# Kernel optimization log

Hardware: AMD Instinct MI355X
Metric: run time of the kernel (lower is better)

Reference implementation:

```python
import jax, jax.numpy as jnp
import numpy as np

# dims
B, H, W = 2, 128, 256
MD = 34            # model_dim (last 2 channels = sin/cos lat)
LD = MD - 2        # learnable_dim = 32
NH, HD = 4, 8      # n_heads, head_dim
SH = 64            # shared_hidden (DISCO out channels)
K = 25             # number of DISCO basis functions (5x5 kernel_shape)
P = 7              # local stencil width (lat x lon support of geodesic basis)
R = P // 2
FF1, FF2 = 512, 256


def setup_inputs() -> dict:
    key = jax.random.key(0)
    ks = jax.random.split(key, 16)
    x = jax.random.normal(ks[0], (B, H, W, MD), dtype=jnp.float32)
    # latitude-dependent sparse geodesic basis values over a 7x7 stencil
    psi_val = jax.random.uniform(ks[1], (K, H, P * P), dtype=jnp.float32) * 0.1
    disco_w = jax.random.normal(ks[2], (SH, K), dtype=jnp.float32) * 0.1
    disco_b = jax.random.normal(ks[3], (SH,), dtype=jnp.float32) * 0.01
    # per-head MLP: shared_hidden -> 32 -> 1
    hw1 = jax.random.normal(ks[4], (NH, SH, 32), dtype=jnp.float32) * (1.0 / np.sqrt(SH))
    hb1 = jax.random.normal(ks[5], (NH, 32), dtype=jnp.float32) * 0.01
    hw2 = jax.random.normal(ks[6], (NH, 32, 1), dtype=jnp.float32) * (1.0 / np.sqrt(32))
    hb2 = jax.random.normal(ks[7], (NH, 1), dtype=jnp.float32) * 0.01
    # FFN: model_dim -> 512 -> 256 -> learnable_dim
    fw1 = jax.random.normal(ks[8], (MD, FF1), dtype=jnp.float32) * (1.0 / np.sqrt(MD))
    fw1 = fw1.at[-2:, :].set(0.0)  # matches ffn[0].weight[:, -2:] = 0 init
    fb1 = jax.random.normal(ks[9], (FF1,), dtype=jnp.float32) * 0.01
    fw2 = jax.random.normal(ks[10], (FF1, FF2), dtype=jnp.float32) * (1.0 / np.sqrt(FF1))
    fb2 = jax.random.normal(ks[11], (FF2,), dtype=jnp.float32) * 0.01
    fw3 = jax.random.normal(ks[12], (FF2, LD), dtype=jnp.float32) * (1.0 / np.sqrt(FF2))
    fb3 = jax.random.normal(ks[13], (LD,), dtype=jnp.float32) * 0.01
    return {"x": x, "psi_val": psi_val, "disco_w": disco_w, "disco_b": disco_b,
            "hw1": hw1, "hb1": hb1, "hw2": hw2, "hb2": hb2,
            "fw1": fw1, "fb1": fb1, "fw2": fw2, "fb2": fb2, "fw3": fw3, "fb3": fb3}


def _gelu(t):
    return jax.nn.gelu(t, approximate=False)  # torch nn.GELU default (erf)


def _disco_s2(xn, psi_val, disco_w, disco_b):
    """DISCO sparse-basis conv on single-channel maps.
    xn: (N, H, W). Basis values vary with output latitude, longitude is
    translation-invariant; support is a lat-clamped / lon-wrapped 7x7 stencil.
    Returns (N, SH, H, W)."""
    xp = jnp.pad(xn, ((0, 0), (R, R), (0, 0)), mode="edge")  # clamp at poles
    shifts = []
    for dlat in range(P):
        row = xp[:, dlat:dlat + H, :]
        for dlon in range(-R, R + 1):
            shifts.append(jnp.roll(row, -dlon, axis=2))  # wrap in longitude
    xs = jnp.stack(shifts, axis=1)  # (N, P*P, H, W)
    basis = jnp.einsum("khp,nphw->nkhw", psi_val, xs)       # basis aggregation
    return jnp.einsum("fk,nkhw->nfhw", disco_w, basis) + disco_b[None, :, None, None]


def reference(x, psi_val, disco_w, disco_b, hw1, hb1, hw2, hb2,
              fw1, fb1, fw2, fb2, fw3, fb3):
    x_learn = x[..., :LD]
    sin_cos = x[..., LD:]
    x_res = x_learn
    # (B,H,W,LD) -> (B*LD, H, W): each learnable channel is a 1-channel map
    xn = x_learn.transpose(0, 3, 1, 2).reshape(B * LD, H, W)
    d = _disco_s2(xn, psi_val, disco_w, disco_b)              # (B*LD, SH, H, W)
    d = d.reshape(B, LD, SH, H, W).transpose(0, 3, 4, 1, 2)    # (B,H,W,LD,SH)
    # per-head MLP over its head_dim slice (head index is outer in LD)
    d = d.reshape(B, H, W, NH, HD, SH)
    h = _gelu(jnp.einsum("bxynds,nso->bxyndo", d, hw1) + hb1[None, None, None, :, None, :])
    h = jnp.einsum("bxyndo,noe->bxynde", h, hw2) + hb2[None, None, None, :, None, :]
    x_learn = h[..., 0].reshape(B, H, W, LD)
    x_learn = x_learn + x_res                                  # use_residual
    x_full = jnp.concatenate([x_learn, sin_cos], axis=-1)
    x_res2 = x_learn
    t = _gelu(x_full @ fw1 + fb1)
    t = _gelu(t @ fw2 + fb2)
    t = t @ fw3 + fb3                                          # dropout p=0 -> id
    x_learn = t + x_res2
    return jnp.concatenate([x_learn, sin_cos], axis=-1)
```

## Files before the change

### kernel.cpp

```cpp
#include <hip/hip_runtime.h>
#include <math.h>


typedef __attribute__((ext_vector_type(8))) short bfrag;
typedef __attribute__((ext_vector_type(4))) float ffrag;
typedef __attribute__((ext_vector_type(4))) short short4v;

union bfi4 { int4 i; bfrag b; };

__device__ __forceinline__ float gelu_f(float v) {
  const float z = v * (2.3022077484f + 0.1029451564f * v * v);
  const float e = __builtin_amdgcn_exp2f(-z);
  return v * __builtin_amdgcn_rcpf(1.0f + e);
}

__device__ __forceinline__ short f2bf(float f) {
  union { float f; unsigned u; } v; v.f = f;
  unsigned r = (v.u + 0x7fffu + ((v.u >> 16) & 1u)) >> 16;
  return (short)r;
}

__device__ __forceinline__ short f2bf_fast(float f) {
  union { float f; unsigned u; } v; v.f = f;
  return (short)((v.u + 0x8000u) >> 16);
}

__device__ __forceinline__ float bf2f(short s) {
  union { float f; unsigned u; } v;
  v.u = ((unsigned)(unsigned short)s) << 16;
  return v.f;
}

__device__ __forceinline__ int pkbf(float a, float b) {
  union { float f; unsigned u; } va, vb; va.f = a; vb.f = b;
  return (int)__builtin_amdgcn_perm(vb.u + 0x8000u, va.u + 0x8000u, 0x07060302u);
}

template <int CTRL>
__device__ __forceinline__ float dpp_add(float v) {
  union { float f; int i; } s, t;
  s.f = v;
  t.i = __builtin_amdgcn_update_dpp(0, s.i, CTRL, 0xf, 0xf, true);
  return v + t.f;
}
__device__ __forceinline__ float reduce16(float v) {
  v = dpp_add<0xB1>(v);
  v = dpp_add<0x4E>(v);
  v = dpp_add<0x141>(v);
  v = dpp_add<0x140>(v);
  return v;
}

__device__ __forceinline__ void st4bf(short* p, float4 v) {
  short4v s;
  s[0] = f2bf(v.x); s[1] = f2bf(v.y); s[2] = f2bf(v.z); s[3] = f2bf(v.w);
  *(short4v*)p = s;
}

__global__ __launch_bounds__(256) void k01_prep(
    const float* __restrict__ psi, const float* __restrict__ dw,
    const float* __restrict__ db,
    const float* __restrict__ fw1, const float* __restrict__ fw2,
    const float* __restrict__ fw3, const float* __restrict__ hw1,
    const float* __restrict__ hb1,
    short* __restrict__ wcb, short* __restrict__ fw1s,
    short* __restrict__ fw2s, short* __restrict__ fw3s,
    short* __restrict__ hw1b, float* __restrict__ hb1e) {
  __shared__ __align__(16) char sm[33280];
  const int bid = blockIdx.x;
  const int tid = threadIdx.x;

  if (bid < 128) {
    short* tile = (short*)sm;
    const int h = bid;
    const int lane = tid & 63;
    const int w = __builtin_amdgcn_readfirstlane(tid >> 6);
    float dwreg[25];
#pragma unroll
    for (int kk = 0; kk < 25; ++kk) dwreg[kk] = dw[lane * 25 + kk];
    const int p0 = w * 13;
    const int pend = (p0 + 13 < 49) ? (p0 + 13) : 49;
#pragma unroll 1
    for (int p = p0; p < pend; ++p) {
      float acc = 0.f;
#pragma unroll
      for (int kk = 0; kk < 25; ++kk)
        acc += dwreg[kk] * psi[kk * 6272 + h * 49 + p];
      tile[lane * 52 + p] = f2bf(acc);
    }
    __syncthreads();
    short* outp = wcb + h * 8192;
    for (int idx = tid; idx < 8192; idx += 256) {
      const int jj = idx & 7, ln = (idx >> 3) & 63;
      const int nt = (idx >> 9) & 3, kt = (idx >> 11) & 1, par = idx >> 12;
      const int k = kt * 32 + (ln >> 4) * 8 + jj;
      const int f = nt * 16 + (ln & 15);
      const int r = k >> 3, dlt = k & 7;
      const int j = par ? (dlt - 1) : dlt;
      short v = 0;
      if (r < 7 && j >= 0 && j < 7) v = tile[f * 52 + r * 7 + j];
      outp[idx] = v;
    }
    return;
  }

  if (bid < 144) {
    short* S = (short*)sm;
    const int kt = bid - 128;
    const float* src = fw2 + kt * 8192;
    for (int q = tid; q < 2048; q += 256) {
      const int lin = q * 4;
      const int kk = lin >> 8, nn = lin & 255;
      st4bf(S + kk * 260 + nn, *(const float4*)(src + lin));
    }
    __syncthreads();
    short* dst = fw2s + kt * 8192;
    for (int q = tid; q < 8192; q += 256) {
      const int jj = q & 7, lane = (q >> 3) & 63, nt = q >> 9;
      const int kk = (lane >> 4) * 8 + jj, nn = nt * 16 + (lane & 15);
      dst[q] = S[kk * 260 + nn];
    }
    return;
  }

  if (bid == 144) {
    short* S = (short*)sm;
    for (int q = tid; q < 4096; q += 256) {
      const int lin = q * 4;
      const int kk = lin >> 9, nn = lin & 511;
      st4bf(S + kk * 516 + nn, *(const float4*)(fw1 + lin));
    }
    __syncthreads();
    for (int q = tid; q < 16384; q += 256) {
      const int jj = q & 7, lane = (q >> 3) & 63, nt = q >> 9;
      const int kk = (lane >> 4) * 8 + jj, nn = nt * 16 + (lane & 15);
      fw1s[q] = S[kk * 516 + nn];
    }
    return;
  }

  if (bid == 145) {
    short* S = (short*)sm;
    for (int q = tid; q < 2048; q += 256) {
      const int lin = q * 4;
      const int kk = lin >> 5, nn = lin & 31;
      st4bf(S + kk * 36 + nn, *(const float4*)(fw3 + lin));
    }
    __syncthreads();
    for (int q = tid; q < 8192; q += 256) {
      const int jj = q & 7, lane = (q >> 3) & 63;
      const int nt = (q >> 9) & 1, kt = q >> 10;
      const int kk = kt * 32 + (lane >> 4) * 8 + jj, nn = nt * 16 + (lane & 15);
      fw3s[q] = S[kk * 36 + nn];
    }
    return;
  }

  if (bid == 146) {
    short* S = (short*)sm;
    for (int q = tid; q < 2048; q += 256) {
      const int lin = q * 4;
      const int row = lin >> 5, nn = lin & 31;
      st4bf(S + row * 36 + nn, *(const float4*)(hw1 + lin));
    }
    __syncthreads();
    for (int q = tid; q < 8192; q += 256) {
      const int jj = q & 7, lane = (q >> 3) & 63;
      const int fr = (q >> 9) & 3, hd = q >> 11;
      const int kt = fr >> 1, nt = fr & 1;
      const int s = kt * 32 + (lane >> 4) * 8 + jj;
      const int forig = (s & 3) * 16 + (s >> 2);
      const int o = nt * 16 + (lane & 15);
      hw1b[q] = S[(hd * 64 + forig) * 36 + o];
    }
    return;
  }

  if (tid < 128) {
    const int n = tid >> 5, o = tid & 31;
    float acc = hb1[n * 32 + o];
#pragma unroll
    for (int s = 0; s < 64; ++s)
      acc += hw1[n * 2048 + s * 32 + o] * db[s];
    hb1e[tid] = acc;
  }
}

__global__ __launch_bounds__(256, 4) void k23_fused(
    const float* __restrict__ x,    const short* __restrict__ wcb,
    const short* __restrict__ hw1b, const float* __restrict__ hb1e,
    const float* __restrict__ hw2,  const float* __restrict__ hb2,
    const short* __restrict__ fw1s, const short* __restrict__ fw2s,
    const short* __restrict__ fw3s,
    const float* __restrict__ fb1,  const float* __restrict__ fb2,
    const float* __restrict__ fb3,  float* __restrict__ outb) {
  __shared__ __align__(16) char smem[36224];
  short* sX = (short*)smem;
  short* sM = (short*)(smem + 34048);

  const int tid = threadIdx.x;
  const int w0  = blockIdx.x * 32;
  const int h   = blockIdx.y;
  const int b   = blockIdx.z;

  {
    int4* p = (int4*)sX;
    int4 z; z.x = z.y = z.z = z.w = 0;
    for (int e = tid; e < (32 * 388) / 8; e += 256) p[e] = z;
  }
  __syncthreads();

#pragma unroll 1
  for (int r = 0; r < 7; ++r) {
    int hr = h - 3 + r; hr = hr < 0 ? 0 : (hr > 127 ? 127 : hr);
    const float* __restrict__ xrow = x + (size_t)((b * 128 + hr) * 256) * 34;
    short* __restrict__ sxr = sX + r * 48;
    for (int e = tid; e < 39 * 16; e += 256) {
      const int c2 = e & 15;
      const int wp = e >> 4;
      const int wr = (w0 - 3 + wp) & 255;
      const float2 v = *(const float2*)&xrow[wr * 34 + c2 * 2];
      short* dp = sxr + (c2 * 2) * 388 + wp;
      dp[0]   = f2bf_fast(v.x);
      dp[388] = f2bf_fast(v.y);
    }
  }

  if (tid < 64) {
    const int wl = tid >> 1;
    const int sc = tid & 1;
    const int idx = ((b * 128 + h) * 256 + (w0 + wl)) * 34 + 32 + sc;
    outb[idx] = x[idx];
  }
  __syncthreads();

  const int lane = tid & 63, lm = lane & 15, lq = lane >> 4;
  const int n = tid >> 6;

  float hb1v[2], hw2v[2];
#pragma unroll
  for (int nt = 0; nt < 2; ++nt) {
    hb1v[nt] = hb1e[n * 32 + nt * 16 + lm];
    hw2v[nt] = hw2[n * 32 + nt * 16 + lm];
  }
  const float hb2n = hb2[n];

  bfrag cB[2][2][4];
#pragma unroll
  for (int par = 0; par < 2; ++par)
#pragma unroll
    for (int kt = 0; kt < 2; ++kt)
#pragma unroll
      for (int nt = 0; nt < 4; ++nt)
        cB[par][kt][nt] = *(const bfrag*)(wcb + h * 8192 +
                            ((par * 2 + kt) * 4 + nt) * 512 + lane * 8);
  bfrag mB[2][2];
#pragma unroll
  for (int kt = 0; kt < 2; ++kt)
#pragma unroll
    for (int nt = 0; nt < 2; ++nt)
      mB[kt][nt] = *(const bfrag*)(hw1b + n * 2048 + (kt * 2 + nt) * 512 + lane * 8);

  short* sDw = (short*)(smem + 24832) + n * 1152;
  const int* tpB = (const int*)sX;

#pragma unroll 1
  for (int i = 0; i < 8; ++i) {
    const int c = n * 8 + i;

    const int base0 = c * 194 + lq * 24 + lm;
    bfi4 u0, u1;
    u0.i.x = tpB[base0];      u0.i.y = tpB[base0 + 1];
    u0.i.z = tpB[base0 + 2];  u0.i.w = tpB[base0 + 3];
    u1.i.x = tpB[base0 + 96]; u1.i.y = tpB[base0 + 97];
    u1.i.z = tpB[base0 + 98]; u1.i.w = tpB[base0 + 99];

#pragma unroll
    for (int par = 0; par < 2; ++par) {
      ffrag dacc[4];
#pragma unroll
      for (int nt = 0; nt < 4; ++nt) dacc[nt] = ffrag{0.f, 0.f, 0.f, 0.f};
#pragma unroll
      for (int nt = 0; nt < 4; ++nt) {
        dacc[nt] = __builtin_amdgcn_mfma_f32_16x16x32_bf16(u0.b, cB[par][0][nt], dacc[nt], 0, 0, 0);
        dacc[nt] = __builtin_amdgcn_mfma_f32_16x16x32_bf16(u1.b, cB[par][1][nt], dacc[nt], 0, 0, 0);
      }

#pragma unroll
      for (int rr = 0; rr < 4; ++rr) {
        int2 w;
        w.x = pkbf(dacc[0][rr], dacc[1][rr]);
        w.y = pkbf(dacc[2][rr], dacc[3][rr]);
        *(int2*)(sDw + (lq * 4 + rr) * 72 + lm * 4) = w;
      }

      bfrag a10 = *(const bfrag*)(sDw + lm * 72 + lq * 8);
      bfrag a11 = *(const bfrag*)(sDw + lm * 72 + 32 + lq * 8);
      ffrag h10 = {0.f, 0.f, 0.f, 0.f}, h11 = {0.f, 0.f, 0.f, 0.f};
      h10 = __builtin_amdgcn_mfma_f32_16x16x32_bf16(a10, mB[0][0], h10, 0, 0, 0);
      h10 = __builtin_amdgcn_mfma_f32_16x16x32_bf16(a11, mB[1][0], h10, 0, 0, 0);
      h11 = __builtin_amdgcn_mfma_f32_16x16x32_bf16(a10, mB[0][1], h11, 0, 0, 0);
      h11 = __builtin_amdgcn_mfma_f32_16x16x32_bf16(a11, mB[1][1], h11, 0, 0, 0);

#pragma unroll
      for (int rr = 0; rr < 4; ++rr) {
        float v = gelu_f(h10[rr] + hb1v[0]) * hw2v[0] +
                  gelu_f(h11[rr] + hb1v[1]) * hw2v[1];
        v = reduce16(v);
        const int p = 2 * (lq * 4 + rr) + par;
        const float res = bf2f(sX[c * 388 + 144 + 3 + p]);
        if (lm == 0) sM[p * 34 + c] = f2bf_fast(v + hb2n + res);
      }
    }
  }
  __syncthreads();

  short* sT1h = (short*)smem;
  short* sT2  = (short*)(smem + 16896);
  const int wave = n;
  const int koff = lq * 8;
  const int mt3 = wave & 1;
  const int nt3 = wave >> 1;
  const int col3 = nt3 * 16 + lm;
  const int pixg = (b * 128 + h) * 256 + w0;

  bfrag aF[2];
#pragma unroll
  for (int mt = 0; mt < 2; ++mt)
    aF[mt] = *(const bfrag*)(sM + (mt * 16 + lm) * 34 + koff);
  float res3[4];
#pragma unroll
  for (int r = 0; r < 4; ++r)
    res3[r] = bf2f(sM[(mt3 * 16 + lq * 4 + r) * 34 + col3]);

  const int n0 = wave * 4;
  ffrag acc[2][4];
#pragma unroll
  for (int mt = 0; mt < 2; ++mt)
#pragma unroll
    for (int ni = 0; ni < 4; ++ni) acc[mt][ni] = ffrag{0.f, 0.f, 0.f, 0.f};
  const short* w2base = fw2s + n0 * 512 + lane * 8;

#pragma unroll 1
  for (int H = 0; H < 2; ++H) {
    bfrag b1f[4];
#pragma unroll
    for (int ni = 0; ni < 4; ++ni)
      b1f[ni] = *(const bfrag*)(fw1s + (H * 16 + wave * 4 + ni) * 512 + lane * 8);
#pragma unroll
    for (int ni = 0; ni < 4; ++ni) {
      const int ntl = wave * 4 + ni;
#pragma unroll
      for (int mt = 0; mt < 2; ++mt) {
        ffrag cc = {0.f, 0.f, 0.f, 0.f};
        cc = __builtin_amdgcn_mfma_f32_16x16x32_bf16(aF[mt], b1f[ni], cc, 0, 0, 0);
        const int colg = H * 256 + ntl * 16 + lm;
        const float bias = fb1[colg];
#pragma unroll
        for (int r = 0; r < 4; ++r) {
          const int row = mt * 16 + lq * 4 + r;
          sT1h[row * 264 + ntl * 16 + lm] = f2bf_fast(gelu_f(cc[r] + bias));
        }
      }
    }
    __syncthreads();

#pragma unroll 2
    for (int kt = 0; kt < 8; ++kt) {
      bfrag bv[4];
#pragma unroll
      for (int ni = 0; ni < 4; ++ni)
        bv[ni] = *(const bfrag*)(w2base + (H * 8 + kt) * 8192 + ni * 512);
      const bfrag a0 = *(const bfrag*)(sT1h + lm * 264 + kt * 32 + koff);
      const bfrag a1 = *(const bfrag*)(sT1h + (16 + lm) * 264 + kt * 32 + koff);
#pragma unroll
      for (int ni = 0; ni < 4; ++ni) {
        acc[0][ni] = __builtin_amdgcn_mfma_f32_16x16x32_bf16(a0, bv[ni], acc[0][ni], 0, 0, 0);
        acc[1][ni] = __builtin_amdgcn_mfma_f32_16x16x32_bf16(a1, bv[ni], acc[1][ni], 0, 0, 0);
      }
    }
    __syncthreads();
  }

#pragma unroll
  for (int mt = 0; mt < 2; ++mt)
#pragma unroll
    for (int ni = 0; ni < 4; ++ni) {
      const int col = (n0 + ni) * 16 + lm;
      const float bias = fb2[col];
#pragma unroll
      for (int r = 0; r < 4; ++r) {
        const int row = mt * 16 + lq * 4 + r;
        sT2[row * 264 + col] = f2bf_fast(gelu_f(acc[mt][ni][r] + bias));
      }
    }
  __syncthreads();

  ffrag c3 = {0.f, 0.f, 0.f, 0.f};
  const short* sA3 = sT2 + (mt3 * 16 + lm) * 264 + koff;
#pragma unroll
  for (int kt = 0; kt < 8; ++kt) {
    const bfrag a = *(const bfrag*)(sA3 + kt * 32);
    const bfrag bw = *(const bfrag*)(fw3s + nt3 * 512 + kt * 1024 + lane * 8);
    c3 = __builtin_amdgcn_mfma_f32_16x16x32_bf16(a, bw, c3, 0, 0, 0);
  }
  {
    const float bias = fb3[col3];
#pragma unroll
    for (int r = 0; r < 4; ++r) {
      const int row = mt3 * 16 + lq * 4 + r;
      outb[(pixg + row) * 34 + col3] = c3[r] + bias + res3[r];
    }
  }
}

extern "C" void kernel_launch(void* const* d_in, const int* in_sizes, int n_in,
                              void* d_out, int out_size, void* d_ws, size_t ws_size,
                              hipStream_t stream) {
  const float* x   = (const float*)d_in[0];
  const float* psi = (const float*)d_in[1];
  const float* dw  = (const float*)d_in[2];
  const float* db  = (const float*)d_in[3];
  const float* hw1 = (const float*)d_in[4];
  const float* hb1 = (const float*)d_in[5];
  const float* hw2 = (const float*)d_in[6];
  const float* hb2 = (const float*)d_in[7];
  const float* fw1 = (const float*)d_in[8];
  const float* fb1 = (const float*)d_in[9];
  const float* fw2 = (const float*)d_in[10];
  const float* fb2 = (const float*)d_in[11];
  const float* fw3 = (const float*)d_in[12];
  const float* fb3 = (const float*)d_in[13];
  float* outb = (float*)d_out;

  short* wcb  = (short*)d_ws;
  short* fw1s = wcb + 1048576;
  short* fw2s = fw1s + 16384;
  short* fw3s = fw2s + 131072;
  short* hw1b = fw3s + 8192;
  float* hb1e = (float*)(hw1b + 8192);

  hipLaunchKernelGGL(k01_prep, dim3(148), dim3(256), 0, stream,
                     psi, dw, db, fw1, fw2, fw3, hw1, hb1,
                     wcb, fw1s, fw2s, fw3s, hw1b, hb1e);
  hipLaunchKernelGGL(k23_fused, dim3(8, 128, 2), dim3(256), 0, stream,
                     x, wcb, hw1b, hb1e, hw2, hb2,
                     fw1s, fw2s, fw3s, fb1, fb2, fb3, outb);
}
```

Before: 170.3 us.

## Fold DISCO weights and per-head first MLP layer into one combined stencil matrix

```diff
diff --git a/kernel.cpp b/kernel.cpp
--- a/kernel.cpp
+++ b/kernel.cpp
@@ -29,11 +29,6 @@
   union { float f; unsigned u; } v;
   v.u = ((unsigned)(unsigned short)s) << 16;
   return v.f;
-}
-
-__device__ __forceinline__ int pkbf(float a, float b) {
-  union { float f; unsigned u; } va, vb; va.f = a; vb.f = b;
-  return (int)__builtin_amdgcn_perm(vb.u + 0x8000u, va.u + 0x8000u, 0x07060302u);
 }
 
 template <int CTRL>
@@ -63,43 +58,46 @@
     const float* __restrict__ fw1, const float* __restrict__ fw2,
     const float* __restrict__ fw3, const float* __restrict__ hw1,
     const float* __restrict__ hb1,
-    short* __restrict__ wcb, short* __restrict__ fw1s,
+    short* __restrict__ w2b, short* __restrict__ fw1s,
     short* __restrict__ fw2s, short* __restrict__ fw3s,
-    short* __restrict__ hw1b, float* __restrict__ hb1e) {
+    float* __restrict__ hb1e) {
   __shared__ __align__(16) char sm[33280];
   const int bid = blockIdx.x;
   const int tid = threadIdx.x;
 
   if (bid < 128) {
-    short* tile = (short*)sm;
-    const int h = bid;
-    const int lane = tid & 63;
-    const int w = __builtin_amdgcn_readfirstlane(tid >> 6);
-    float dwreg[25];
-#pragma unroll
-    for (int kk = 0; kk < 25; ++kk) dwreg[kk] = dw[lane * 25 + kk];
-    const int p0 = w * 13;
-    const int pend = (p0 + 13 < 49) ? (p0 + 13) : 49;
+    const int h  = bid;
+    const int no = tid & 127;
+    const int ph = tid >> 7;
+    float hv[64];
+#pragma unroll
+    for (int s = 0; s < 64; ++s)
+      hv[s] = hw1[(no >> 5) * 2048 + s * 32 + (no & 31)];
+    float G[25];
+#pragma unroll
+    for (int kk = 0; kk < 25; ++kk) {
+      float a = 0.f;
+#pragma unroll
+      for (int s = 0; s < 64; ++s) a += hv[s] * dw[s * 25 + kk];
+      G[kk] = a;
+    }
+    short* outp = w2b + h * 16384;
+    const float* psih = psi + h * 49;
 #pragma unroll 1
-    for (int p = p0; p < pend; ++p) {
+    for (int pk = ph * 64; pk < ph * 64 + 64; ++pk) {
+      const int par = pk >> 6, k = pk & 63;
+      const int r = k >> 3, dlt = k & 7;
+      const int j = dlt - par;
       float acc = 0.f;
-#pragma unroll
-      for (int kk = 0; kk < 25; ++kk)
-        acc += dwreg[kk] * psi[kk * 6272 + h * 49 + p];
-      tile[lane * 52 + p] = f2bf(acc);
-    }
-    __syncthreads();
-    short* outp = wcb + h * 8192;
-    for (int idx = tid; idx < 8192; idx += 256) {
-      const int jj = idx & 7, ln = (idx >> 3) & 63;
-      const int nt = (idx >> 9) & 3, kt = (idx >> 11) & 1, par = idx >> 12;
-      const int k = kt * 32 + (ln >> 4) * 8 + jj;
-      const int f = nt * 16 + (ln & 15);
-      const int r = k >> 3, dlt = k & 7;
-      const int j = par ? (dlt - 1) : dlt;
-      short v = 0;
-      if (r < 7 && j >= 0 && j < 7) v = tile[f * 52 + r * 7 + j];
-      outp[idx] = v;
+      if (r < 7 && j >= 0 && j < 7) {
+        const int tap = r * 7 + j;
+#pragma unroll
+        for (int kk = 0; kk < 25; ++kk)
+          acc += G[kk] * psih[kk * 6272 + tap];
+      }
+      const int kt = k >> 5, kq = (k >> 3) & 3, jj = k & 7;
+      const int fi = (par * 2 + kt) * 8 + (no >> 4);
+      outp[fi * 512 + (kq * 16 + (no & 15)) * 8 + jj] = f2bf(acc);
     }
     return;
   }
@@ -156,26 +154,6 @@
     return;
   }
 
-  if (bid == 146) {
-    short* S = (short*)sm;
-    for (int q = tid; q < 2048; q += 256) {
-      const int lin = q * 4;
-      const int row = lin >> 5, nn = lin & 31;
-      st4bf(S + row * 36 + nn, *(const float4*)(hw1 + lin));
-    }
-    __syncthreads();
-    for (int q = tid; q < 8192; q += 256) {
-      const int jj = q & 7, lane = (q >> 3) & 63;
-      const int fr = (q >> 9) & 3, hd = q >> 11;
-      const int kt = fr >> 1, nt = fr & 1;
-      const int s = kt * 32 + (lane >> 4) * 8 + jj;
-      const int forig = (s & 3) * 16 + (s >> 2);
-      const int o = nt * 16 + (lane & 15);
-      hw1b[q] = S[(hd * 64 + forig) * 36 + o];
-    }
-    return;
-  }
-
   if (tid < 128) {
     const int n = tid >> 5, o = tid & 31;
     float acc = hb1[n * 32 + o];
@@ -187,9 +165,9 @@
 }
 
 __global__ __launch_bounds__(256, 4) void k23_fused(
-    const float* __restrict__ x,    const short* __restrict__ wcb,
-    const short* __restrict__ hw1b, const float* __restrict__ hb1e,
-    const float* __restrict__ hw2,  const float* __restrict__ hb2,
+    const float* __restrict__ x,    const short* __restrict__ w2b,
+    const float* __restrict__ hb1e, const float* __restrict__ hw2,
+    const float* __restrict__ hb2,
     const short* __restrict__ fw1s, const short* __restrict__ fw2s,
     const short* __restrict__ fw3s,
     const float* __restrict__ fb1,  const float* __restrict__ fb2,
@@ -245,23 +223,16 @@
   }
   const float hb2n = hb2[n];
 
-  bfrag cB[2][2][4];
+  bfrag cB2[2][2][2];
 #pragma unroll
   for (int par = 0; par < 2; ++par)
 #pragma unroll
     for (int kt = 0; kt < 2; ++kt)
 #pragma unroll
-      for (int nt = 0; nt < 4; ++nt)
-        cB[par][kt][nt] = *(const bfrag*)(wcb + h * 8192 +
-                            ((par * 2 + kt) * 4 + nt) * 512 + lane * 8);
-  bfrag mB[2][2];
-#pragma unroll
-  for (int kt = 0; kt < 2; ++kt)
-#pragma unroll
-    for (int nt = 0; nt < 2; ++nt)
-      mB[kt][nt] = *(const bfrag*)(hw1b + n * 2048 + (kt * 2 + nt) * 512 + lane * 8);
-
-  short* sDw = (short*)(smem + 24832) + n * 1152;
+      for (int nt = 0; nt < 2; ++nt)
+        cB2[par][kt][nt] = *(const bfrag*)(w2b + h * 16384 +
+                            ((par * 2 + kt) * 8 + (n * 2 + nt)) * 512 + lane * 8);
+
   const int* tpB = (const int*)sX;
 
 #pragma unroll 1
@@ -277,35 +248,16 @@
 
 #pragma unroll
     for (int par = 0; par < 2; ++par) {
-      ffrag dacc[4];
-#pragma unroll
-      for (int nt = 0; nt < 4; ++nt) dacc[nt] = ffrag{0.f, 0.f, 0.f, 0.f};
-#pragma unroll
-      for (int nt = 0; nt < 4; ++nt) {
-        dacc[nt] = __builtin_amdgcn_mfma_f32_16x16x32_bf16(u0.b, cB[par][0][nt], dacc[nt], 0, 0, 0);
-        dacc[nt] = __builtin_amdgcn_mfma_f32_16x16x32_bf16(u1.b, cB[par][1][nt], dacc[nt], 0, 0, 0);
-      }
+      ffrag h1a = {0.f, 0.f, 0.f, 0.f}, h1b = {0.f, 0.f, 0.f, 0.f};
+      h1a = __builtin_amdgcn_mfma_f32_16x16x32_bf16(u0.b, cB2[par][0][0], h1a, 0, 0, 0);
+      h1a = __builtin_amdgcn_mfma_f32_16x16x32_bf16(u1.b, cB2[par][1][0], h1a, 0, 0, 0);
+      h1b = __builtin_amdgcn_mfma_f32_16x16x32_bf16(u0.b, cB2[par][0][1], h1b, 0, 0, 0);
+      h1b = __builtin_amdgcn_mfma_f32_16x16x32_bf16(u1.b, cB2[par][1][1], h1b, 0, 0, 0);
 
 #pragma unroll
       for (int rr = 0; rr < 4; ++rr) {
-        int2 w;
-        w.x = pkbf(dacc[0][rr], dacc[1][rr]);
-        w.y = pkbf(dacc[2][rr], dacc[3][rr]);
-        *(int2*)(sDw + (lq * 4 + rr) * 72 + lm * 4) = w;
-      }
-
-      bfrag a10 = *(const bfrag*)(sDw + lm * 72 + lq * 8);
-      bfrag a11 = *(const bfrag*)(sDw + lm * 72 + 32 + lq * 8);
-      ffrag h10 = {0.f, 0.f, 0.f, 0.f}, h11 = {0.f, 0.f, 0.f, 0.f};
-      h10 = __builtin_amdgcn_mfma_f32_16x16x32_bf16(a10, mB[0][0], h10, 0, 0, 0);
-      h10 = __builtin_amdgcn_mfma_f32_16x16x32_bf16(a11, mB[1][0], h10, 0, 0, 0);
-      h11 = __builtin_amdgcn_mfma_f32_16x16x32_bf16(a10, mB[0][1], h11, 0, 0, 0);
-      h11 = __builtin_amdgcn_mfma_f32_16x16x32_bf16(a11, mB[1][1], h11, 0, 0, 0);
-
-#pragma unroll
-      for (int rr = 0; rr < 4; ++rr) {
-        float v = gelu_f(h10[rr] + hb1v[0]) * hw2v[0] +
-                  gelu_f(h11[rr] + hb1v[1]) * hw2v[1];
+        float v = gelu_f(h1a[rr] + hb1v[0]) * hw2v[0] +
+                  gelu_f(h1b[rr] + hb1v[1]) * hw2v[1];
         v = reduce16(v);
         const int p = 2 * (lq * 4 + rr) + par;
         const float res = bf2f(sX[c * 388 + 144 + 3 + p]);
@@ -433,17 +385,16 @@
   const float* fb3 = (const float*)d_in[13];
   float* outb = (float*)d_out;
 
-  short* wcb  = (short*)d_ws;
-  short* fw1s = wcb + 1048576;
+  short* w2b  = (short*)d_ws;
+  short* fw1s = w2b + 2097152;
   short* fw2s = fw1s + 16384;
   short* fw3s = fw2s + 131072;
-  short* hw1b = fw3s + 8192;
-  float* hb1e = (float*)(hw1b + 8192);
-
-  hipLaunchKernelGGL(k01_prep, dim3(148), dim3(256), 0, stream,
+  float* hb1e = (float*)(fw3s + 8192);
+
+  hipLaunchKernelGGL(k01_prep, dim3(147), dim3(256), 0, stream,
                      psi, dw, db, fw1, fw2, fw3, hw1, hb1,
-                     wcb, fw1s, fw2s, fw3s, hw1b, hb1e);
+                     w2b, fw1s, fw2s, fw3s, hb1e);
   hipLaunchKernelGGL(k23_fused, dim3(8, 128, 2), dim3(256), 0, stream,
-                     x, wcb, hw1b, hb1e, hw2, hb2,
+                     x, w2b, hb1e, hw2, hb2,
                      fw1s, fw2s, fw3s, fb1, fb2, fb3, outb);
 }
```

Result: slower. 214.1 us (+25.7%).
